# Kernel optimization log

Hardware: AMD Instinct MI355X
Metric: run time of the kernel (lower is better)

## Reference

```python
import jax, jax.numpy as jnp
import numpy as np

N_NODES = 50000
N_EDGES = 800000
D_FEAT = 128
HIDDEN = 128
N_CLASSES = 40


def setup_inputs() -> dict:
    key = jax.random.key(0)
    ks = jax.random.split(key, 8)
    s = 1.0 / np.sqrt(D_FEAT)
    return {
        "x": jax.random.normal(ks[0], (N_NODES, D_FEAT), jnp.float32),
        "edge_index": jax.random.randint(ks[1], (2, N_EDGES), 0, N_NODES, jnp.int64),
        "Wl0": jax.random.normal(ks[2], (D_FEAT, HIDDEN), jnp.float32) * s,
        "bl0": jnp.zeros((HIDDEN,), jnp.float32),
        "Wr0": jax.random.normal(ks[3], (D_FEAT, HIDDEN), jnp.float32) * s,
        "Wl1": jax.random.normal(ks[4], (HIDDEN, HIDDEN), jnp.float32) * s,
        "bl1": jnp.zeros((HIDDEN,), jnp.float32),
        "Wr1": jax.random.normal(ks[5], (HIDDEN, HIDDEN), jnp.float32) * s,
        "Wl2": jax.random.normal(ks[6], (HIDDEN, N_CLASSES), jnp.float32) * s,
        "bl2": jnp.zeros((N_CLASSES,), jnp.float32),
        "Wr2": jax.random.normal(ks[7], (HIDDEN, N_CLASSES), jnp.float32) * s,
    }


def _sage_conv(x, src, dst, Wl, bl, Wr):
    # PyG SAGEConv (mean aggr): out = lin_l(mean_{j in N(i)} x_j) + lin_r(x_i)
    msg_sum = jax.ops.segment_sum(x[src], dst, num_segments=N_NODES)  # [N, d]
    deg = jax.ops.segment_sum(jnp.ones((src.shape[0],), x.dtype), dst, num_segments=N_NODES)
    mean = msg_sum / jnp.clip(deg, 1.0)[:, None]
    return mean @ Wl + bl + x @ Wr


def reference(x, edge_index, Wl0, bl0, Wr0, Wl1, bl1, Wr1, Wl2, bl2, Wr2):
    src, dst = edge_index[0], edge_index[1]
    h = jax.nn.relu(_sage_conv(x, src, dst, Wl0, bl0, Wr0))
    h = jax.nn.relu(_sage_conv(h, src, dst, Wl1, bl1, Wr1))
    h = jax.nn.relu(_sage_conv(h, src, dst, Wl2, bl2, Wr2))
    # dropout is identity in eval mode
    return jax.nn.log_softmax(h, axis=1)
```

## Files before the change

### kernel.cpp

```cpp
#include <hip/hip_runtime.h>
#include <cstdint>
#include <cstddef>
#include <cmath>

#define N_NODES 50000
#define N_EDGES 800000
#define D_FEAT 128
#define HIDDEN 128
#define N_CLASSES 40

typedef _Float16 half8 __attribute__((ext_vector_type(8)));
typedef _Float16 half4 __attribute__((ext_vector_type(4)));
typedef float f32x4 __attribute__((ext_vector_type(4)));


__global__ __launch_bounds__(256) void k_deg(const int* __restrict__ dst, int* __restrict__ deg,
                                             unsigned short* __restrict__ rank) {
    int e = blockIdx.x * 256 + threadIdx.x;
    if (e < N_EDGES) {
        int r = atomicAdd(&deg[dst[e]], 1);
        rank[e] = (unsigned short)r;
    }
}

__global__ __launch_bounds__(1024) void k_scan1(const int* __restrict__ deg, int* __restrict__ offsets,
                                                int* __restrict__ partials) {
    __shared__ int wsums[16];
    int tid = threadIdx.x;
    int g = blockIdx.x * 1024 + tid;
    int v = (g < N_NODES) ? deg[g] : 0;
    int lane = tid & 63;
    int wid = tid >> 6;
    int incl = v;
    #pragma unroll
    for (int off = 1; off < 64; off <<= 1) {
        int t = __shfl_up(incl, off);
        if (lane >= off) incl += t;
    }
    if (lane == 63) wsums[wid] = incl;
    __syncthreads();
    if (wid == 0) {
        int wv = (lane < 16) ? wsums[lane] : 0;
        int wincl = wv;
        #pragma unroll
        for (int off = 1; off < 16; off <<= 1) {
            int t = __shfl_up(wincl, off);
            if (lane >= off) wincl += t;
        }
        if (lane < 16) wsums[lane] = wincl - wv;
    }
    __syncthreads();
    if (g < N_NODES) offsets[g] = wsums[wid] + incl - v;
    if (tid == 1023) partials[blockIdx.x] = wsums[15] + incl;
}

__global__ __launch_bounds__(64) void k_scan2(int* __restrict__ partials, int nParts) {
    int lane = threadIdx.x;
    int v = (lane < nParts) ? partials[lane] : 0;
    int incl = v;
    #pragma unroll
    for (int off = 1; off < 64; off <<= 1) {
        int t = __shfl_up(incl, off);
        if (lane >= off) incl += t;
    }
    if (lane < nParts) partials[lane] = incl - v;
}

__global__ __launch_bounds__(256) void k_scan3(int* __restrict__ offsets, const int* __restrict__ partials) {
    int g = blockIdx.x * 256 + threadIdx.x;
    if (g < N_NODES) offsets[g] += partials[g >> 10];
}

__global__ __launch_bounds__(256) void k_scatter(const int* __restrict__ src, const int* __restrict__ dst,
                                                 const int* __restrict__ offsets,
                                                 const unsigned short* __restrict__ rank,
                                                 unsigned short* __restrict__ sorted_src) {
    int e = blockIdx.x * 256 + threadIdx.x;
    if (e < N_EDGES) {
        int d = dst[e];
        int pos = offsets[d] + (int)rank[e];
        sorted_src[pos] = (unsigned short)src[e];
    }
}


#define CVT_BLOCKS 6250

__global__ __launch_bounds__(256) void k_prep(const float* __restrict__ x, _Float16* __restrict__ xh,
                                              const float* __restrict__ Wl0, const float* __restrict__ Wr0, _Float16* __restrict__ Wc0,
                                              const float* __restrict__ Wl1, const float* __restrict__ Wr1, _Float16* __restrict__ Wc1,
                                              const float* __restrict__ Wl2, const float* __restrict__ Wr2, _Float16* __restrict__ Wc2) {
    int bid = blockIdx.x;
    if (bid < CVT_BLOCKS) {
        int i = bid * 256 + threadIdx.x;
        float4 v = *(const float4*)(x + (size_t)i * 4);
        half4 o;
        o[0] = (_Float16)v.x; o[1] = (_Float16)v.y; o[2] = (_Float16)v.z; o[3] = (_Float16)v.w;
        *(half4*)(xh + (size_t)i * 4) = o;
        return;
    }
    bid -= CVT_BLOCKS;
    const float* Wl; const float* Wr; _Float16* dst; int NF, Nout, cell0;
    if (bid < 16)      { Wl = Wl0; Wr = Wr0; dst = Wc0; NF = 8; Nout = 128; cell0 = bid * 4; }
    else if (bid < 32) { Wl = Wl1; Wr = Wr1; dst = Wc1; NF = 8; Nout = 128; cell0 = (bid - 16) * 4; }
    else               { Wl = Wl2; Wr = Wr2; dst = Wc2; NF = 3; Nout = 40;  cell0 = (bid - 32) * 4; }
    int cell = cell0 + (threadIdx.x >> 6);
    int t = cell / NF;
    int f = cell % NF;
    int l = threadIdx.x & 63;
    int kb = t * 32 + (l >> 4) * 8;
    int n = f * 16 + (l & 15);
    half8 v;
    #pragma unroll
    for (int i = 0; i < 8; ++i) {
        int k = kb + i;
        float w = 0.f;
        if (n < Nout) w = (k < 128) ? Wl[k * Nout + n] : Wr[(k - 128) * Nout + n];
        v[i] = (_Float16)w;
    }
    *(half8*)(dst + ((size_t)cell * 64 + l) * 8) = v;
}


__global__ __launch_bounds__(256) void k_agg_h(const _Float16* __restrict__ feat, const int* __restrict__ offsets,
                                               const int* __restrict__ deg,
                                               const unsigned short* __restrict__ sorted_src,
                                               _Float16* __restrict__ mean) {
    int wave = (int)((blockIdx.x * 256 + threadIdx.x) >> 6);
    int lane = threadIdx.x & 63;
    if (wave >= N_NODES) return;
    int start = offsets[wave];
    int cnt = deg[wave];
    int grp = lane >> 4;
    int cl = lane & 15;
    float acc[8] = {0.f, 0.f, 0.f, 0.f, 0.f, 0.f, 0.f, 0.f};
    #pragma unroll 4
    for (int i = 0; i < cnt; i += 4) {
        int e = i + grp;
        if (e < cnt) {
            int s = (int)sorted_src[start + e];
            half8 v = *(const half8*)(feat + (size_t)s * 128 + cl * 8);
            #pragma unroll
            for (int j = 0; j < 8; ++j) acc[j] += (float)v[j];
        }
    }
    #pragma unroll
    for (int j = 0; j < 8; ++j) {
        acc[j] += __shfl_xor(acc[j], 16);
        acc[j] += __shfl_xor(acc[j], 32);
    }
    if (grp == 0) {
        float r = 1.0f / (float)(cnt > 0 ? cnt : 1);
        half8 o;
        #pragma unroll
        for (int j = 0; j < 8; ++j) o[j] = (_Float16)(acc[j] * r);
        *(half8*)(mean + (size_t)wave * 128 + cl * 8) = o;
    }
}


__global__ __launch_bounds__(256) void k_gemm_h(const _Float16* __restrict__ A, const _Float16* __restrict__ B,
                                                const _Float16* __restrict__ Wc, const float* __restrict__ bias,
                                                _Float16* __restrict__ outp) {
    __shared__ _Float16 sA[128 * 128];
    __shared__ _Float16 sB[128 * 128];
    int tid = threadIdx.x;
    int rows0 = blockIdx.x * 128;
    for (int i = 0; i < 8; ++i) {
        int cid = i * 256 + tid;
        int r = cid >> 4;
        int ch = cid & 15;
        int gr = rows0 + r;
        int grc = gr < N_NODES ? gr : N_NODES - 1;
        half8 va = *(const half8*)(A + (size_t)grc * 128 + ch * 8);
        half8 vb = *(const half8*)(B + (size_t)grc * 128 + ch * 8);
        int sch = ch ^ (r & 15);
        *(half8*)(sA + r * 128 + sch * 8) = va;
        *(half8*)(sB + r * 128 + sch * 8) = vb;
    }
    __syncthreads();
    int w = tid >> 6;
    int lane = tid & 63;
    int ln = lane & 15, lg = lane >> 4;
    int r0 = w * 32 + ln;
    int r1 = r0 + 16;
    f32x4 acc[2][8];
    #pragma unroll
    for (int i = 0; i < 2; ++i)
        #pragma unroll
        for (int f = 0; f < 8; ++f) acc[i][f] = (f32x4){0.f, 0.f, 0.f, 0.f};
    #pragma unroll
    for (int t = 0; t < 8; ++t) {
        const _Float16* P = (t < 4) ? sA : sB;
        int ch = (t & 3) * 4 + lg;
        half8 a0 = *(const half8*)(P + r0 * 128 + (ch ^ (r0 & 15)) * 8);
        half8 a1 = *(const half8*)(P + r1 * 128 + (ch ^ (r1 & 15)) * 8);
        #pragma unroll
        for (int f = 0; f < 8; ++f) {
            half8 b = *(const half8*)(Wc + ((size_t)(t * 8 + f) * 64 + lane) * 8);
            acc[0][f] = __builtin_amdgcn_mfma_f32_16x16x32_f16(a0, b, acc[0][f], 0, 0, 0);
            acc[1][f] = __builtin_amdgcn_mfma_f32_16x16x32_f16(a1, b, acc[1][f], 0, 0, 0);
        }
    }
    int rw = rows0 + w * 32;
    #pragma unroll
    for (int mf = 0; mf < 2; ++mf) {
        #pragma unroll
        for (int f = 0; f < 8; ++f) {
            int n = f * 16 + ln;
            float bv = bias[n];
            #pragma unroll
            for (int r = 0; r < 4; ++r) {
                int m = rw + mf * 16 + lg * 4 + r;
                if (m < N_NODES) {
                    float v = fmaxf(acc[mf][f][r] + bv, 0.f);
                    outp[(size_t)m * 128 + n] = (_Float16)v;
                }
            }
        }
    }
}


__global__ __launch_bounds__(256) void k_gemm_f(const _Float16* __restrict__ A, const _Float16* __restrict__ B,
                                                const _Float16* __restrict__ Wc, const float* __restrict__ bias,
                                                float* __restrict__ outp) {
    __shared__ _Float16 sA[128 * 128];
    __shared__ _Float16 sB[128 * 128];
    int tid = threadIdx.x;
    int rows0 = blockIdx.x * 128;
    for (int i = 0; i < 8; ++i) {
        int cid = i * 256 + tid;
        int r = cid >> 4;
        int ch = cid & 15;
        int gr = rows0 + r;
        int grc = gr < N_NODES ? gr : N_NODES - 1;
        half8 va = *(const half8*)(A + (size_t)grc * 128 + ch * 8);
        half8 vb = *(const half8*)(B + (size_t)grc * 128 + ch * 8);
        int sch = ch ^ (r & 15);
        *(half8*)(sA + r * 128 + sch * 8) = va;
        *(half8*)(sB + r * 128 + sch * 8) = vb;
    }
    __syncthreads();
    int w = tid >> 6;
    int lane = tid & 63;
    int ln = lane & 15, lg = lane >> 4;
    int r0 = w * 32 + ln;
    int r1 = r0 + 16;
    f32x4 acc[2][3];
    #pragma unroll
    for (int i = 0; i < 2; ++i)
        #pragma unroll
        for (int f = 0; f < 3; ++f) acc[i][f] = (f32x4){0.f, 0.f, 0.f, 0.f};
    #pragma unroll
    for (int t = 0; t < 8; ++t) {
        const _Float16* P = (t < 4) ? sA : sB;
        int ch = (t & 3) * 4 + lg;
        half8 a0 = *(const half8*)(P + r0 * 128 + (ch ^ (r0 & 15)) * 8);
        half8 a1 = *(const half8*)(P + r1 * 128 + (ch ^ (r1 & 15)) * 8);
        #pragma unroll
        for (int f = 0; f < 3; ++f) {
            half8 b = *(const half8*)(Wc + ((size_t)(t * 3 + f) * 64 + lane) * 8);
            acc[0][f] = __builtin_amdgcn_mfma_f32_16x16x32_f16(a0, b, acc[0][f], 0, 0, 0);
            acc[1][f] = __builtin_amdgcn_mfma_f32_16x16x32_f16(a1, b, acc[1][f], 0, 0, 0);
        }
    }
    float bv[3];
    #pragma unroll
    for (int f = 0; f < 3; ++f) {
        int n = f * 16 + ln;
        bv[f] = (n < N_CLASSES) ? bias[n] : 0.f;
    }
    int rw = rows0 + w * 32;
    #pragma unroll
    for (int mf = 0; mf < 2; ++mf) {
        #pragma unroll
        for (int r = 0; r < 4; ++r) {
            int m = rw + mf * 16 + lg * 4 + r;
            float v[3];
            float vmax = -INFINITY;
            #pragma unroll
            for (int f = 0; f < 3; ++f) {
                int n = f * 16 + ln;
                v[f] = fmaxf(acc[mf][f][r] + bv[f], 0.f);
                if (n < N_CLASSES) vmax = fmaxf(vmax, v[f]);
            }
            #pragma unroll
            for (int off = 1; off < 16; off <<= 1) vmax = fmaxf(vmax, __shfl_xor(vmax, off));
            float s = 0.f;
            #pragma unroll
            for (int f = 0; f < 3; ++f) {
                int n = f * 16 + ln;
                if (n < N_CLASSES) s += expf(v[f] - vmax);
            }
            #pragma unroll
            for (int off = 1; off < 16; off <<= 1) s += __shfl_xor(s, off);
            float lse = vmax + logf(s);
            if (m < N_NODES) {
                #pragma unroll
                for (int f = 0; f < 3; ++f) {
                    int n = f * 16 + ln;
                    if (n < N_CLASSES) outp[(size_t)m * N_CLASSES + n] = v[f] - lse;
                }
            }
        }
    }
}

extern "C" void kernel_launch(void* const* d_in, const int* in_sizes, int n_in,
                              void* d_out, int out_size, void* d_ws, size_t ws_size,
                              hipStream_t stream) {
    const float* x   = (const float*)d_in[0];
    const int*   ei  = (const int*)d_in[1];
    const float* Wl0 = (const float*)d_in[2];
    const float* bl0 = (const float*)d_in[3];
    const float* Wr0 = (const float*)d_in[4];
    const float* Wl1 = (const float*)d_in[5];
    const float* bl1 = (const float*)d_in[6];
    const float* Wr1 = (const float*)d_in[7];
    const float* Wl2 = (const float*)d_in[8];
    const float* bl2 = (const float*)d_in[9];
    const float* Wr2 = (const float*)d_in[10];
    float* out = (float*)d_out;

    const int* src = ei;
    const int* dst = ei + N_EDGES;

    int* offsets  = (int*)d_ws;
    int* deg      = offsets + 50016;
    int* partials = deg + 50016;
    unsigned short* rank   = (unsigned short*)(partials + 64);
    unsigned short* sorted = rank + N_EDGES;
    _Float16* xh  = (_Float16*)(sorted + N_EDGES);
    _Float16* mh  = xh + (size_t)N_NODES * 128;
    _Float16* h0  = mh + (size_t)N_NODES * 128;
    _Float16* h1  = h0 + (size_t)N_NODES * 128;
    _Float16* Wc0 = h1 + (size_t)N_NODES * 128;
    _Float16* Wc1 = Wc0 + 8 * 8 * 64 * 8;
    _Float16* Wc2 = Wc1 + 8 * 8 * 64 * 8;

    hipMemsetAsync(deg, 0, 50016 * sizeof(int), stream);

    const int edgeBlocks = (N_EDGES + 255) / 256;
    const int scanBlocks = (N_NODES + 1023) / 1024;
    k_deg<<<edgeBlocks, 256, 0, stream>>>(dst, deg, rank);
    k_scan1<<<scanBlocks, 1024, 0, stream>>>(deg, offsets, partials);
    k_scan2<<<1, 64, 0, stream>>>(partials, scanBlocks);
    k_scan3<<<(N_NODES + 255) / 256, 256, 0, stream>>>(offsets, partials);
    k_scatter<<<edgeBlocks, 256, 0, stream>>>(src, dst, offsets, rank, sorted);

    k_prep<<<CVT_BLOCKS + 38, 256, 0, stream>>>(x, xh, Wl0, Wr0, Wc0, Wl1, Wr1, Wc1, Wl2, Wr2, Wc2);

    const int waveBlocks = (N_NODES * 64 + 255) / 256;
    const int gemmBlocks = (N_NODES + 127) / 128;

    k_agg_h<<<waveBlocks, 256, 0, stream>>>(xh, offsets, deg, sorted, mh);
    k_gemm_h<<<gemmBlocks, 256, 0, stream>>>(mh, xh, Wc0, bl0, h0);
    k_agg_h<<<waveBlocks, 256, 0, stream>>>(h0, offsets, deg, sorted, mh);
    k_gemm_h<<<gemmBlocks, 256, 0, stream>>>(mh, h0, Wc1, bl1, h1);
    k_agg_h<<<waveBlocks, 256, 0, stream>>>(h1, offsets, deg, sorted, mh);
    k_gemm_f<<<gemmBlocks, 256, 0, stream>>>(mh, h1, Wc2, bl2, out);
}
```

Before: 309.8 us.

## Fuse neighbor aggregation into per-layer GEMM kernels and merge setup kernels

Each SAGE layer becomes a single kernel: the block gathers and averages neighbor features for its 128 rows straight into shared memory, then runs the MFMA GEMM, so the intermediate mean buffer is never written to or read from global memory. The degree-count kernel is merged with the feature and weight conversion kernel. The scan's third pass is removed by adding the block partial sum where offsets are read. The trade-off is far fewer waves (391 blocks of 8 waves, each wave handling 16 nodes one after another), which reduces latency hiding for the irregular gather loads.

```diff
diff --git a/kernel.cpp b/kernel.cpp
--- a/kernel.cpp
+++ b/kernel.cpp
@@ -13,15 +13,54 @@
 typedef _Float16 half4 __attribute__((ext_vector_type(4)));
 typedef float f32x4 __attribute__((ext_vector_type(4)));
 
-
-__global__ __launch_bounds__(256) void k_deg(const int* __restrict__ dst, int* __restrict__ deg,
-                                             unsigned short* __restrict__ rank) {
-    int e = blockIdx.x * 256 + threadIdx.x;
-    if (e < N_EDGES) {
+#define EDGE_BLOCKS 3125
+#define CVT_BLOCKS 6250
+
+
+__global__ __launch_bounds__(256) void k_build(const int* __restrict__ dst, int* __restrict__ deg,
+                                               unsigned short* __restrict__ rank,
+                                               const float* __restrict__ x, _Float16* __restrict__ xh,
+                                               const float* __restrict__ Wl0, const float* __restrict__ Wr0, _Float16* __restrict__ Wc0,
+                                               const float* __restrict__ Wl1, const float* __restrict__ Wr1, _Float16* __restrict__ Wc1,
+                                               const float* __restrict__ Wl2, const float* __restrict__ Wr2, _Float16* __restrict__ Wc2) {
+    int bid = blockIdx.x;
+    if (bid < EDGE_BLOCKS) {
+        int e = bid * 256 + threadIdx.x;
         int r = atomicAdd(&deg[dst[e]], 1);
         rank[e] = (unsigned short)r;
-    }
-}
+        return;
+    }
+    bid -= EDGE_BLOCKS;
+    if (bid < CVT_BLOCKS) {
+        int i = bid * 256 + threadIdx.x;
+        float4 v = *(const float4*)(x + (size_t)i * 4);
+        half4 o;
+        o[0] = (_Float16)v.x; o[1] = (_Float16)v.y; o[2] = (_Float16)v.z; o[3] = (_Float16)v.w;
+        *(half4*)(xh + (size_t)i * 4) = o;
+        return;
+    }
+    bid -= CVT_BLOCKS;
+    const float* Wl; const float* Wr; _Float16* dstw; int NF, Nout, cell0;
+    if (bid < 16)      { Wl = Wl0; Wr = Wr0; dstw = Wc0; NF = 8; Nout = 128; cell0 = bid * 4; }
+    else if (bid < 32) { Wl = Wl1; Wr = Wr1; dstw = Wc1; NF = 8; Nout = 128; cell0 = (bid - 16) * 4; }
+    else               { Wl = Wl2; Wr = Wr2; dstw = Wc2; NF = 3; Nout = 40;  cell0 = (bid - 32) * 4; }
+    int cell = cell0 + (threadIdx.x >> 6);
+    int t = cell / NF;
+    int f = cell % NF;
+    int l = threadIdx.x & 63;
+    int kb = t * 32 + (l >> 4) * 8;
+    int n = f * 16 + (l & 15);
+    half8 v;
+    #pragma unroll
+    for (int i = 0; i < 8; ++i) {
+        int k = kb + i;
+        float w = 0.f;
+        if (n < Nout) w = (k < 128) ? Wl[k * Nout + n] : Wr[(k - 128) * Nout + n];
+        v[i] = (_Float16)w;
+    }
+    *(half8*)(dstw + ((size_t)cell * 64 + l) * 8) = v;
+}
+
 
 __global__ __launch_bounds__(1024) void k_scan1(const int* __restrict__ deg, int* __restrict__ offsets,
                                                 int* __restrict__ partials) {
@@ -66,203 +105,156 @@
     if (lane < nParts) partials[lane] = incl - v;
 }
 
-__global__ __launch_bounds__(256) void k_scan3(int* __restrict__ offsets, const int* __restrict__ partials) {
-    int g = blockIdx.x * 256 + threadIdx.x;
-    if (g < N_NODES) offsets[g] += partials[g >> 10];
-}
-
 __global__ __launch_bounds__(256) void k_scatter(const int* __restrict__ src, const int* __restrict__ dst,
-                                                 const int* __restrict__ offsets,
+                                                 const int* __restrict__ offsets, const int* __restrict__ partials,
                                                  const unsigned short* __restrict__ rank,
                                                  unsigned short* __restrict__ sorted_src) {
     int e = blockIdx.x * 256 + threadIdx.x;
     if (e < N_EDGES) {
         int d = dst[e];
-        int pos = offsets[d] + (int)rank[e];
+        int pos = offsets[d] + partials[d >> 10] + (int)rank[e];
         sorted_src[pos] = (unsigned short)src[e];
     }
 }
 
 
-#define CVT_BLOCKS 6250
-
-__global__ __launch_bounds__(256) void k_prep(const float* __restrict__ x, _Float16* __restrict__ xh,
-                                              const float* __restrict__ Wl0, const float* __restrict__ Wr0, _Float16* __restrict__ Wc0,
-                                              const float* __restrict__ Wl1, const float* __restrict__ Wr1, _Float16* __restrict__ Wc1,
-                                              const float* __restrict__ Wl2, const float* __restrict__ Wr2, _Float16* __restrict__ Wc2) {
-    int bid = blockIdx.x;
-    if (bid < CVT_BLOCKS) {
-        int i = bid * 256 + threadIdx.x;
-        float4 v = *(const float4*)(x + (size_t)i * 4);
-        half4 o;
-        o[0] = (_Float16)v.x; o[1] = (_Float16)v.y; o[2] = (_Float16)v.z; o[3] = (_Float16)v.w;
-        *(half4*)(xh + (size_t)i * 4) = o;
-        return;
-    }
-    bid -= CVT_BLOCKS;
-    const float* Wl; const float* Wr; _Float16* dst; int NF, Nout, cell0;
-    if (bid < 16)      { Wl = Wl0; Wr = Wr0; dst = Wc0; NF = 8; Nout = 128; cell0 = bid * 4; }
-    else if (bid < 32) { Wl = Wl1; Wr = Wr1; dst = Wc1; NF = 8; Nout = 128; cell0 = (bid - 16) * 4; }
-    else               { Wl = Wl2; Wr = Wr2; dst = Wc2; NF = 3; Nout = 40;  cell0 = (bid - 32) * 4; }
-    int cell = cell0 + (threadIdx.x >> 6);
-    int t = cell / NF;
-    int f = cell % NF;
-    int l = threadIdx.x & 63;
-    int kb = t * 32 + (l >> 4) * 8;
-    int n = f * 16 + (l & 15);
-    half8 v;
-    #pragma unroll
-    for (int i = 0; i < 8; ++i) {
-        int k = kb + i;
-        float w = 0.f;
-        if (n < Nout) w = (k < 128) ? Wl[k * Nout + n] : Wr[(k - 128) * Nout + n];
-        v[i] = (_Float16)w;
-    }
-    *(half8*)(dst + ((size_t)cell * 64 + l) * 8) = v;
-}
-
-
-__global__ __launch_bounds__(256) void k_agg_h(const _Float16* __restrict__ feat, const int* __restrict__ offsets,
-                                               const int* __restrict__ deg,
-                                               const unsigned short* __restrict__ sorted_src,
-                                               _Float16* __restrict__ mean) {
-    int wave = (int)((blockIdx.x * 256 + threadIdx.x) >> 6);
-    int lane = threadIdx.x & 63;
-    if (wave >= N_NODES) return;
-    int start = offsets[wave];
-    int cnt = deg[wave];
-    int grp = lane >> 4;
-    int cl = lane & 15;
-    float acc[8] = {0.f, 0.f, 0.f, 0.f, 0.f, 0.f, 0.f, 0.f};
-    #pragma unroll 4
-    for (int i = 0; i < cnt; i += 4) {
-        int e = i + grp;
-        if (e < cnt) {
-            int s = (int)sorted_src[start + e];
-            half8 v = *(const half8*)(feat + (size_t)s * 128 + cl * 8);
+__device__ __forceinline__ void agg_into_lds(const _Float16* __restrict__ feat, const int* __restrict__ offsets,
+                                             const int* __restrict__ partials, const int* __restrict__ deg,
+                                             const unsigned short* __restrict__ sorted_src,
+                                             _Float16* sA, int rows0, int tid) {
+    int w = tid >> 6, lane = tid & 63;
+    int grp = lane >> 4, cl = lane & 15;
+    for (int j = 0; j < 16; ++j) {
+        int r = w * 16 + j;
+        int node = rows0 + r;
+        float acc[8] = {0.f, 0.f, 0.f, 0.f, 0.f, 0.f, 0.f, 0.f};
+        int cnt = 0;
+        if (node < N_NODES) {
+            int start = offsets[node] + partials[node >> 10];
+            cnt = deg[node];
+            int i = 0;
+            int nfull = cnt & ~7;
+            for (; i < nfull; i += 8) {
+                int s0 = (int)sorted_src[start + i + grp];
+                int s1 = (int)sorted_src[start + i + 4 + grp];
+                half8 v0 = *(const half8*)(feat + (size_t)s0 * 128 + cl * 8);
+                half8 v1 = *(const half8*)(feat + (size_t)s1 * 128 + cl * 8);
+                #pragma unroll
+                for (int q = 0; q < 8; ++q) acc[q] += (float)v0[q] + (float)v1[q];
+            }
+            for (; i < cnt; i += 4) {
+                int e = i + grp;
+                if (e < cnt) {
+                    int s = (int)sorted_src[start + e];
+                    half8 v = *(const half8*)(feat + (size_t)s * 128 + cl * 8);
+                    #pragma unroll
+                    for (int q = 0; q < 8; ++q) acc[q] += (float)v[q];
+                }
+            }
+        }
+        #pragma unroll
+        for (int q = 0; q < 8; ++q) {
+            acc[q] += __shfl_xor(acc[q], 16);
+            acc[q] += __shfl_xor(acc[q], 32);
+        }
+        if (grp == 0) {
+            float rs = 1.0f / (float)(cnt > 0 ? cnt : 1);
+            half8 o;
             #pragma unroll
-            for (int j = 0; j < 8; ++j) acc[j] += (float)v[j];
-        }
-    }
-    #pragma unroll
-    for (int j = 0; j < 8; ++j) {
-        acc[j] += __shfl_xor(acc[j], 16);
-        acc[j] += __shfl_xor(acc[j], 32);
-    }
-    if (grp == 0) {
-        float r = 1.0f / (float)(cnt > 0 ? cnt : 1);
-        half8 o;
-        #pragma unroll
-        for (int j = 0; j < 8; ++j) o[j] = (_Float16)(acc[j] * r);
-        *(half8*)(mean + (size_t)wave * 128 + cl * 8) = o;
-    }
-}
-
-
-__global__ __launch_bounds__(256) void k_gemm_h(const _Float16* __restrict__ A, const _Float16* __restrict__ B,
-                                                const _Float16* __restrict__ Wc, const float* __restrict__ bias,
-                                                _Float16* __restrict__ outp) {
+            for (int q = 0; q < 8; ++q) o[q] = (_Float16)(acc[q] * rs);
+            *(half8*)(sA + r * 128 + (cl ^ (r & 15)) * 8) = o;
+        }
+    }
+}
+
+__global__ __launch_bounds__(512) void k_layer_h(const _Float16* __restrict__ feat, const int* __restrict__ offsets,
+                                                 const int* __restrict__ partials, const int* __restrict__ deg,
+                                                 const unsigned short* __restrict__ sorted_src,
+                                                 const _Float16* __restrict__ Wc, const float* __restrict__ bias,
+                                                 _Float16* __restrict__ outp) {
     __shared__ _Float16 sA[128 * 128];
     __shared__ _Float16 sB[128 * 128];
     int tid = threadIdx.x;
     int rows0 = blockIdx.x * 128;
-    for (int i = 0; i < 8; ++i) {
-        int cid = i * 256 + tid;
-        int r = cid >> 4;
-        int ch = cid & 15;
+    #pragma unroll
+    for (int i = 0; i < 4; ++i) {
+        int cid = i * 512 + tid;
+        int r = cid >> 4, ch = cid & 15;
         int gr = rows0 + r;
         int grc = gr < N_NODES ? gr : N_NODES - 1;
-        half8 va = *(const half8*)(A + (size_t)grc * 128 + ch * 8);
-        half8 vb = *(const half8*)(B + (size_t)grc * 128 + ch * 8);
-        int sch = ch ^ (r & 15);
-        *(half8*)(sA + r * 128 + sch * 8) = va;
-        *(half8*)(sB + r * 128 + sch * 8) = vb;
-    }
+        half8 v = *(const half8*)(feat + (size_t)grc * 128 + ch * 8);
+        *(half8*)(sB + r * 128 + (ch ^ (r & 15)) * 8) = v;
+    }
+    agg_into_lds(feat, offsets, partials, deg, sorted_src, sA, rows0, tid);
     __syncthreads();
-    int w = tid >> 6;
-    int lane = tid & 63;
+    int w = tid >> 6, lane = tid & 63;
     int ln = lane & 15, lg = lane >> 4;
-    int r0 = w * 32 + ln;
-    int r1 = r0 + 16;
-    f32x4 acc[2][8];
-    #pragma unroll
-    for (int i = 0; i < 2; ++i)
-        #pragma unroll
-        for (int f = 0; f < 8; ++f) acc[i][f] = (f32x4){0.f, 0.f, 0.f, 0.f};
+    int r0 = w * 16 + ln;
+    f32x4 acc[8];
+    #pragma unroll
+    for (int f = 0; f < 8; ++f) acc[f] = (f32x4){0.f, 0.f, 0.f, 0.f};
     #pragma unroll
     for (int t = 0; t < 8; ++t) {
         const _Float16* P = (t < 4) ? sA : sB;
         int ch = (t & 3) * 4 + lg;
-        half8 a0 = *(const half8*)(P + r0 * 128 + (ch ^ (r0 & 15)) * 8);
-        half8 a1 = *(const half8*)(P + r1 * 128 + (ch ^ (r1 & 15)) * 8);
+        half8 a = *(const half8*)(P + r0 * 128 + (ch ^ (r0 & 15)) * 8);
         #pragma unroll
         for (int f = 0; f < 8; ++f) {
             half8 b = *(const half8*)(Wc + ((size_t)(t * 8 + f) * 64 + lane) * 8);
-            acc[0][f] = __builtin_amdgcn_mfma_f32_16x16x32_f16(a0, b, acc[0][f], 0, 0, 0);
-            acc[1][f] = __builtin_amdgcn_mfma_f32_16x16x32_f16(a1, b, acc[1][f], 0, 0, 0);
-        }
-    }
-    int rw = rows0 + w * 32;
-    #pragma unroll
-    for (int mf = 0; mf < 2; ++mf) {
-        #pragma unroll
-        for (int f = 0; f < 8; ++f) {
-            int n = f * 16 + ln;
-            float bv = bias[n];
-            #pragma unroll
-            for (int r = 0; r < 4; ++r) {
-                int m = rw + mf * 16 + lg * 4 + r;
-                if (m < N_NODES) {
-                    float v = fmaxf(acc[mf][f][r] + bv, 0.f);
-                    outp[(size_t)m * 128 + n] = (_Float16)v;
-                }
+            acc[f] = __builtin_amdgcn_mfma_f32_16x16x32_f16(a, b, acc[f], 0, 0, 0);
+        }
+    }
+    int rw = rows0 + w * 16;
+    #pragma unroll
+    for (int f = 0; f < 8; ++f) {
+        int n = f * 16 + ln;
+        float bv = bias[n];
+        #pragma unroll
+        for (int r = 0; r < 4; ++r) {
+            int m = rw + lg * 4 + r;
+            if (m < N_NODES) {
+                float v = fmaxf(acc[f][r] + bv, 0.f);
+                outp[(size_t)m * 128 + n] = (_Float16)v;
             }
         }
     }
 }
 
-
-__global__ __launch_bounds__(256) void k_gemm_f(const _Float16* __restrict__ A, const _Float16* __restrict__ B,
-                                                const _Float16* __restrict__ Wc, const float* __restrict__ bias,
-                                                float* __restrict__ outp) {
+__global__ __launch_bounds__(512) void k_layer_f(const _Float16* __restrict__ feat, const int* __restrict__ offsets,
+                                                 const int* __restrict__ partials, const int* __restrict__ deg,
+                                                 const unsigned short* __restrict__ sorted_src,
+                                                 const _Float16* __restrict__ Wc, const float* __restrict__ bias,
+                                                 float* __restrict__ outp) {
     __shared__ _Float16 sA[128 * 128];
     __shared__ _Float16 sB[128 * 128];
     int tid = threadIdx.x;
     int rows0 = blockIdx.x * 128;
-    for (int i = 0; i < 8; ++i) {
-        int cid = i * 256 + tid;
-        int r = cid >> 4;
-        int ch = cid & 15;
+    #pragma unroll
+    for (int i = 0; i < 4; ++i) {
+        int cid = i * 512 + tid;
+        int r = cid >> 4, ch = cid & 15;
         int gr = rows0 + r;
         int grc = gr < N_NODES ? gr : N_NODES - 1;
-        half8 va = *(const half8*)(A + (size_t)grc * 128 + ch * 8);
-        half8 vb = *(const half8*)(B + (size_t)grc * 128 + ch * 8);
-        int sch = ch ^ (r & 15);
-        *(half8*)(sA + r * 128 + sch * 8) = va;
-        *(half8*)(sB + r * 128 + sch * 8) = vb;
-    }
+        half8 v = *(const half8*)(feat + (size_t)grc * 128 + ch * 8);
+        *(half8*)(sB + r * 128 + (ch ^ (r & 15)) * 8) = v;
+    }
+    agg_into_lds(feat, offsets, partials, deg, sorted_src, sA, rows0, tid);
     __syncthreads();
-    int w = tid >> 6;
-    int lane = tid & 63;
+    int w = tid >> 6, lane = tid & 63;
     int ln = lane & 15, lg = lane >> 4;
-    int r0 = w * 32 + ln;
-    int r1 = r0 + 16;
-    f32x4 acc[2][3];
-    #pragma unroll
-    for (int i = 0; i < 2; ++i)
-        #pragma unroll
-        for (int f = 0; f < 3; ++f) acc[i][f] = (f32x4){0.f, 0.f, 0.f, 0.f};
+    int r0 = w * 16 + ln;
+    f32x4 acc[3];
+    #pragma unroll
+    for (int f = 0; f < 3; ++f) acc[f] = (f32x4){0.f, 0.f, 0.f, 0.f};
     #pragma unroll
     for (int t = 0; t < 8; ++t) {
         const _Float16* P = (t < 4) ? sA : sB;
         int ch = (t & 3) * 4 + lg;
-        half8 a0 = *(const half8*)(P + r0 * 128 + (ch ^ (r0 & 15)) * 8);
-        half8 a1 = *(const half8*)(P + r1 * 128 + (ch ^ (r1 & 15)) * 8);
+        half8 a = *(const half8*)(P + r0 * 128 + (ch ^ (r0 & 15)) * 8);
         #pragma unroll
         for (int f = 0; f < 3; ++f) {
             half8 b = *(const half8*)(Wc + ((size_t)(t * 3 + f) * 64 + lane) * 8);
-            acc[0][f] = __builtin_amdgcn_mfma_f32_16x16x32_f16(a0, b, acc[0][f], 0, 0, 0);
-            acc[1][f] = __builtin_amdgcn_mfma_f32_16x16x32_f16(a1, b, acc[1][f], 0, 0, 0);
+            acc[f] = __builtin_amdgcn_mfma_f32_16x16x32_f16(a, b, acc[f], 0, 0, 0);
         }
     }
     float bv[3];
@@ -271,37 +263,34 @@
         int n = f * 16 + ln;
         bv[f] = (n < N_CLASSES) ? bias[n] : 0.f;
     }
-    int rw = rows0 + w * 32;
-    #pragma unroll
-    for (int mf = 0; mf < 2; ++mf) {
-        #pragma unroll
-        for (int r = 0; r < 4; ++r) {
-            int m = rw + mf * 16 + lg * 4 + r;
-            float v[3];
-            float vmax = -INFINITY;
+    int rw = rows0 + w * 16;
+    #pragma unroll
+    for (int r = 0; r < 4; ++r) {
+        int m = rw + lg * 4 + r;
+        float v[3];
+        float vmax = -INFINITY;
+        #pragma unroll
+        for (int f = 0; f < 3; ++f) {
+            int n = f * 16 + ln;
+            v[f] = fmaxf(acc[f][r] + bv[f], 0.f);
+            if (n < N_CLASSES) vmax = fmaxf(vmax, v[f]);
+        }
+        #pragma unroll
+        for (int off = 1; off < 16; off <<= 1) vmax = fmaxf(vmax, __shfl_xor(vmax, off));
+        float s = 0.f;
+        #pragma unroll
+        for (int f = 0; f < 3; ++f) {
+            int n = f * 16 + ln;
+            if (n < N_CLASSES) s += expf(v[f] - vmax);
+        }
+        #pragma unroll
+        for (int off = 1; off < 16; off <<= 1) s += __shfl_xor(s, off);
+        float lse = vmax + logf(s);
+        if (m < N_NODES) {
             #pragma unroll
             for (int f = 0; f < 3; ++f) {
                 int n = f * 16 + ln;
-                v[f] = fmaxf(acc[mf][f][r] + bv[f], 0.f);
-                if (n < N_CLASSES) vmax = fmaxf(vmax, v[f]);
-            }
-            #pragma unroll
-            for (int off = 1; off < 16; off <<= 1) vmax = fmaxf(vmax, __shfl_xor(vmax, off));
-            float s = 0.f;
-            #pragma unroll
-            for (int f = 0; f < 3; ++f) {
-                int n = f * 16 + ln;
-                if (n < N_CLASSES) s += expf(v[f] - vmax);
-            }
-            #pragma unroll
-            for (int off = 1; off < 16; off <<= 1) s += __shfl_xor(s, off);
-            float lse = vmax + logf(s);
-            if (m < N_NODES) {
-                #pragma unroll
-                for (int f = 0; f < 3; ++f) {
-                    int n = f * 16 + ln;
-                    if (n < N_CLASSES) outp[(size_t)m * N_CLASSES + n] = v[f] - lse;
-                }
+                if (n < N_CLASSES) outp[(size_t)m * N_CLASSES + n] = v[f] - lse;
             }
         }
     }
@@ -332,8 +321,7 @@
     unsigned short* rank   = (unsigned short*)(partials + 64);
     unsigned short* sorted = rank + N_EDGES;
     _Float16* xh  = (_Float16*)(sorted + N_EDGES);
-    _Float16* mh  = xh + (size_t)N_NODES * 128;
-    _Float16* h0  = mh + (size_t)N_NODES * 128;
+    _Float16* h0  = xh + (size_t)N_NODES * 128;
     _Float16* h1  = h0 + (size_t)N_NODES * 128;
     _Float16* Wc0 = h1 + (size_t)N_NODES * 128;
     _Float16* Wc1 = Wc0 + 8 * 8 * 64 * 8;
@@ -341,23 +329,15 @@
 
     hipMemsetAsync(deg, 0, 50016 * sizeof(int), stream);
 
-    const int edgeBlocks = (N_EDGES + 255) / 256;
     const int scanBlocks = (N_NODES + 1023) / 1024;
-    k_deg<<<edgeBlocks, 256, 0, stream>>>(dst, deg, rank);
+    k_build<<<EDGE_BLOCKS + CVT_BLOCKS + 38, 256, 0, stream>>>(dst, deg, rank, x, xh,
+                                                               Wl0, Wr0, Wc0, Wl1, Wr1, Wc1, Wl2, Wr2, Wc2);
     k_scan1<<<scanBlocks, 1024, 0, stream>>>(deg, offsets, partials);
     k_scan2<<<1, 64, 0, stream>>>(partials, scanBlocks);
-    k_scan3<<<(N_NODES + 255) / 256, 256, 0, stream>>>(offsets, partials);
-    k_scatter<<<edgeBlocks, 256, 0, stream>>>(src, dst, offsets, rank, sorted);
-
-    k_prep<<<CVT_BLOCKS + 38, 256, 0, stream>>>(x, xh, Wl0, Wr0, Wc0, Wl1, Wr1, Wc1, Wl2, Wr2, Wc2);
-
-    const int waveBlocks = (N_NODES * 64 + 255) / 256;
-    const int gemmBlocks = (N_NODES + 127) / 128;
-
-    k_agg_h<<<waveBlocks, 256, 0, stream>>>(xh, offsets, deg, sorted, mh);
-    k_gemm_h<<<gemmBlocks, 256, 0, stream>>>(mh, xh, Wc0, bl0, h0);
-    k_agg_h<<<waveBlocks, 256, 0, stream>>>(h0, offsets, deg, sorted, mh);
-    k_gemm_h<<<gemmBlocks, 256, 0, stream>>>(mh, h0, Wc1, bl1, h1);
-    k_agg_h<<<waveBlocks, 256, 0, stream>>>(h1, offsets, deg, sorted, mh);
-    k_gemm_f<<<gemmBlocks, 256, 0, stream>>>(mh, h1, Wc2, bl2, out);
-}
+    k_scatter<<<EDGE_BLOCKS, 256, 0, stream>>>(src, dst, offsets, partials, rank, sorted);
+
+    const int layerBlocks = (N_NODES + 127) / 128;
+    k_layer_h<<<layerBlocks, 512, 0, stream>>>(xh, offsets, partials, deg, sorted, Wc0, bl0, h0);
+    k_layer_h<<<layerBlocks, 512, 0, stream>>>(h0, offsets, partials, deg, sorted, Wc1, bl1, h1);
+    k_layer_f<<<layerBlocks, 512, 0, stream>>>(h1, offsets, partials, deg, sorted, Wc2, bl2, out);
+}
```

After: 321.6 us. 3.8% more time.

## Merge preprocessing kernels, drop scan3, and aggregate with 16 lanes per node

Applied to the files above, without the earlier changes.

Folds the degree-count kernel into the fp16 conversion and weight-packing kernel so one launch does all of them. Removes the scan-fixup kernel by adding the block partial sum wherever offsets are read. Rewrites aggregation so each node gets 16 lanes instead of a full 64-lane wave, iterating edges serially, which removes the cross-group shuffle reduction and the idle wave tails. This cuts launch count and aggregation overhead, but each lane now has less memory-level parallelism per node.

```diff
diff --git a/kernel.cpp b/kernel.cpp
--- a/kernel.cpp
+++ b/kernel.cpp
@@ -13,15 +13,54 @@
 typedef _Float16 half4 __attribute__((ext_vector_type(4)));
 typedef float f32x4 __attribute__((ext_vector_type(4)));
 
-
-__global__ __launch_bounds__(256) void k_deg(const int* __restrict__ dst, int* __restrict__ deg,
-                                             unsigned short* __restrict__ rank) {
-    int e = blockIdx.x * 256 + threadIdx.x;
-    if (e < N_EDGES) {
+#define EDGE_BLOCKS 3125
+#define CVT_BLOCKS 6250
+
+
+__global__ __launch_bounds__(256) void k_build(const int* __restrict__ dst, int* __restrict__ deg,
+                                               unsigned short* __restrict__ rank,
+                                               const float* __restrict__ x, _Float16* __restrict__ xh,
+                                               const float* __restrict__ Wl0, const float* __restrict__ Wr0, _Float16* __restrict__ Wc0,
+                                               const float* __restrict__ Wl1, const float* __restrict__ Wr1, _Float16* __restrict__ Wc1,
+                                               const float* __restrict__ Wl2, const float* __restrict__ Wr2, _Float16* __restrict__ Wc2) {
+    int bid = blockIdx.x;
+    if (bid < EDGE_BLOCKS) {
+        int e = bid * 256 + threadIdx.x;
         int r = atomicAdd(&deg[dst[e]], 1);
         rank[e] = (unsigned short)r;
-    }
-}
+        return;
+    }
+    bid -= EDGE_BLOCKS;
+    if (bid < CVT_BLOCKS) {
+        int i = bid * 256 + threadIdx.x;
+        float4 v = *(const float4*)(x + (size_t)i * 4);
+        half4 o;
+        o[0] = (_Float16)v.x; o[1] = (_Float16)v.y; o[2] = (_Float16)v.z; o[3] = (_Float16)v.w;
+        *(half4*)(xh + (size_t)i * 4) = o;
+        return;
+    }
+    bid -= CVT_BLOCKS;
+    const float* Wl; const float* Wr; _Float16* dstw; int NF, Nout, cell0;
+    if (bid < 16)      { Wl = Wl0; Wr = Wr0; dstw = Wc0; NF = 8; Nout = 128; cell0 = bid * 4; }
+    else if (bid < 32) { Wl = Wl1; Wr = Wr1; dstw = Wc1; NF = 8; Nout = 128; cell0 = (bid - 16) * 4; }
+    else               { Wl = Wl2; Wr = Wr2; dstw = Wc2; NF = 3; Nout = 40;  cell0 = (bid - 32) * 4; }
+    int cell = cell0 + (threadIdx.x >> 6);
+    int t = cell / NF;
+    int f = cell % NF;
+    int l = threadIdx.x & 63;
+    int kb = t * 32 + (l >> 4) * 8;
+    int n = f * 16 + (l & 15);
+    half8 v;
+    #pragma unroll
+    for (int i = 0; i < 8; ++i) {
+        int k = kb + i;
+        float w = 0.f;
+        if (n < Nout) w = (k < 128) ? Wl[k * Nout + n] : Wr[(k - 128) * Nout + n];
+        v[i] = (_Float16)w;
+    }
+    *(half8*)(dstw + ((size_t)cell * 64 + l) * 8) = v;
+}
+
 
 __global__ __launch_bounds__(1024) void k_scan1(const int* __restrict__ deg, int* __restrict__ offsets,
                                                 int* __restrict__ partials) {
@@ -66,96 +105,41 @@
     if (lane < nParts) partials[lane] = incl - v;
 }
 
-__global__ __launch_bounds__(256) void k_scan3(int* __restrict__ offsets, const int* __restrict__ partials) {
-    int g = blockIdx.x * 256 + threadIdx.x;
-    if (g < N_NODES) offsets[g] += partials[g >> 10];
-}
-
 __global__ __launch_bounds__(256) void k_scatter(const int* __restrict__ src, const int* __restrict__ dst,
-                                                 const int* __restrict__ offsets,
+                                                 const int* __restrict__ offsets, const int* __restrict__ partials,
                                                  const unsigned short* __restrict__ rank,
                                                  unsigned short* __restrict__ sorted_src) {
     int e = blockIdx.x * 256 + threadIdx.x;
     if (e < N_EDGES) {
         int d = dst[e];
-        int pos = offsets[d] + (int)rank[e];
+        int pos = offsets[d] + partials[d >> 10] + (int)rank[e];
         sorted_src[pos] = (unsigned short)src[e];
     }
 }
 
 
-#define CVT_BLOCKS 6250
-
-__global__ __launch_bounds__(256) void k_prep(const float* __restrict__ x, _Float16* __restrict__ xh,
-                                              const float* __restrict__ Wl0, const float* __restrict__ Wr0, _Float16* __restrict__ Wc0,
-                                              const float* __restrict__ Wl1, const float* __restrict__ Wr1, _Float16* __restrict__ Wc1,
-                                              const float* __restrict__ Wl2, const float* __restrict__ Wr2, _Float16* __restrict__ Wc2) {
-    int bid = blockIdx.x;
-    if (bid < CVT_BLOCKS) {
-        int i = bid * 256 + threadIdx.x;
-        float4 v = *(const float4*)(x + (size_t)i * 4);
-        half4 o;
-        o[0] = (_Float16)v.x; o[1] = (_Float16)v.y; o[2] = (_Float16)v.z; o[3] = (_Float16)v.w;
-        *(half4*)(xh + (size_t)i * 4) = o;
-        return;
-    }
-    bid -= CVT_BLOCKS;
-    const float* Wl; const float* Wr; _Float16* dst; int NF, Nout, cell0;
-    if (bid < 16)      { Wl = Wl0; Wr = Wr0; dst = Wc0; NF = 8; Nout = 128; cell0 = bid * 4; }
-    else if (bid < 32) { Wl = Wl1; Wr = Wr1; dst = Wc1; NF = 8; Nout = 128; cell0 = (bid - 16) * 4; }
-    else               { Wl = Wl2; Wr = Wr2; dst = Wc2; NF = 3; Nout = 40;  cell0 = (bid - 32) * 4; }
-    int cell = cell0 + (threadIdx.x >> 6);
-    int t = cell / NF;
-    int f = cell % NF;
-    int l = threadIdx.x & 63;
-    int kb = t * 32 + (l >> 4) * 8;
-    int n = f * 16 + (l & 15);
-    half8 v;
-    #pragma unroll
-    for (int i = 0; i < 8; ++i) {
-        int k = kb + i;
-        float w = 0.f;
-        if (n < Nout) w = (k < 128) ? Wl[k * Nout + n] : Wr[(k - 128) * Nout + n];
-        v[i] = (_Float16)w;
-    }
-    *(half8*)(dst + ((size_t)cell * 64 + l) * 8) = v;
-}
-
-
 __global__ __launch_bounds__(256) void k_agg_h(const _Float16* __restrict__ feat, const int* __restrict__ offsets,
-                                               const int* __restrict__ deg,
+                                               const int* __restrict__ partials, const int* __restrict__ deg,
                                                const unsigned short* __restrict__ sorted_src,
                                                _Float16* __restrict__ mean) {
-    int wave = (int)((blockIdx.x * 256 + threadIdx.x) >> 6);
-    int lane = threadIdx.x & 63;
-    if (wave >= N_NODES) return;
-    int start = offsets[wave];
-    int cnt = deg[wave];
-    int grp = lane >> 4;
-    int cl = lane & 15;
+    int node = (int)((blockIdx.x * 256 + threadIdx.x) >> 4);
+    int cl = threadIdx.x & 15;
+    if (node >= N_NODES) return;
+    int start = offsets[node] + partials[node >> 10];
+    int cnt = deg[node];
     float acc[8] = {0.f, 0.f, 0.f, 0.f, 0.f, 0.f, 0.f, 0.f};
     #pragma unroll 4
-    for (int i = 0; i < cnt; i += 4) {
-        int e = i + grp;
-        if (e < cnt) {
-            int s = (int)sorted_src[start + e];
-            half8 v = *(const half8*)(feat + (size_t)s * 128 + cl * 8);
-            #pragma unroll
-            for (int j = 0; j < 8; ++j) acc[j] += (float)v[j];
-        }
-    }
-    #pragma unroll
-    for (int j = 0; j < 8; ++j) {
-        acc[j] += __shfl_xor(acc[j], 16);
-        acc[j] += __shfl_xor(acc[j], 32);
-    }
-    if (grp == 0) {
-        float r = 1.0f / (float)(cnt > 0 ? cnt : 1);
-        half8 o;
-        #pragma unroll
-        for (int j = 0; j < 8; ++j) o[j] = (_Float16)(acc[j] * r);
-        *(half8*)(mean + (size_t)wave * 128 + cl * 8) = o;
-    }
+    for (int e = 0; e < cnt; ++e) {
+        int s = (int)sorted_src[start + e];
+        half8 v = *(const half8*)(feat + (size_t)s * 128 + cl * 8);
+        #pragma unroll
+        for (int q = 0; q < 8; ++q) acc[q] += (float)v[q];
+    }
+    float r = 1.0f / (float)(cnt > 0 ? cnt : 1);
+    half8 o;
+    #pragma unroll
+    for (int q = 0; q < 8; ++q) o[q] = (_Float16)(acc[q] * r);
+    *(half8*)(mean + (size_t)node * 128 + cl * 8) = o;
 }
 
 
@@ -341,23 +325,20 @@
 
     hipMemsetAsync(deg, 0, 50016 * sizeof(int), stream);
 
-    const int edgeBlocks = (N_EDGES + 255) / 256;
     const int scanBlocks = (N_NODES + 1023) / 1024;
-    k_deg<<<edgeBlocks, 256, 0, stream>>>(dst, deg, rank);
+    k_build<<<EDGE_BLOCKS + CVT_BLOCKS + 38, 256, 0, stream>>>(dst, deg, rank, x, xh,
+                                                               Wl0, Wr0, Wc0, Wl1, Wr1, Wc1, Wl2, Wr2, Wc2);
     k_scan1<<<scanBlocks, 1024, 0, stream>>>(deg, offsets, partials);
     k_scan2<<<1, 64, 0, stream>>>(partials, scanBlocks);
-    k_scan3<<<(N_NODES + 255) / 256, 256, 0, stream>>>(offsets, partials);
-    k_scatter<<<edgeBlocks, 256, 0, stream>>>(src, dst, offsets, rank, sorted);
-
-    k_prep<<<CVT_BLOCKS + 38, 256, 0, stream>>>(x, xh, Wl0, Wr0, Wc0, Wl1, Wr1, Wc1, Wl2, Wr2, Wc2);
-
-    const int waveBlocks = (N_NODES * 64 + 255) / 256;
+    k_scatter<<<EDGE_BLOCKS, 256, 0, stream>>>(src, dst, offsets, partials, rank, sorted);
+
+    const int aggBlocks  = (N_NODES * 16 + 255) / 256;
     const int gemmBlocks = (N_NODES + 127) / 128;
 
-    k_agg_h<<<waveBlocks, 256, 0, stream>>>(xh, offsets, deg, sorted, mh);
+    k_agg_h<<<aggBlocks, 256, 0, stream>>>(xh, offsets, partials, deg, sorted, mh);
     k_gemm_h<<<gemmBlocks, 256, 0, stream>>>(mh, xh, Wc0, bl0, h0);
-    k_agg_h<<<waveBlocks, 256, 0, stream>>>(h0, offsets, deg, sorted, mh);
+    k_agg_h<<<aggBlocks, 256, 0, stream>>>(h0, offsets, partials, deg, sorted, mh);
     k_gemm_h<<<gemmBlocks, 256, 0, stream>>>(mh, h0, Wc1, bl1, h1);
-    k_agg_h<<<waveBlocks, 256, 0, stream>>>(h1, offsets, deg, sorted, mh);
+    k_agg_h<<<aggBlocks, 256, 0, stream>>>(h1, offsets, partials, deg, sorted, mh);
     k_gemm_f<<<gemmBlocks, 256, 0, stream>>>(mh, h1, Wc2, bl2, out);
 }
```

Result: faster. 279.1 us (-9.9%).
